# Kernel optimization log

Measured on AMD Instinct MI355X. Metric: run time of the kernel, lower is better.

## Reference

```python
import jax, jax.numpy as jnp
import numpy as np

DIM = 256
HEADS = 8
HEAD_DIM = DIM // HEADS
WS = 7            # window size
SHIFT = 3         # shift size
H = 56
W = 56
B = 32
WA = WS * WS      # window area = 49
NWH, NWW = H // WS, W // WS
NW = NWH * NWW    # windows per image


def _make_attn_mask():
    # replicate the torch mask construction for the shifted windows
    img = np.zeros((H, W), dtype=np.float32)
    cnt = 0
    for hs in (slice(0, -WS), slice(-WS, -SHIFT), slice(-SHIFT, None)):
        for ws_ in (slice(0, -WS), slice(-WS, -SHIFT), slice(-SHIFT, None)):
            img[hs, ws_] = cnt
            cnt += 1
    mw = img.reshape(NWH, WS, NWW, WS).transpose(0, 2, 1, 3).reshape(-1, WA)  # (nW, 49)
    diff = mw[:, None, :] - mw[:, :, None]                                    # (nW, 49, 49)
    return np.where(diff != 0, -100.0, 0.0).astype(np.float32)


def _make_rel_index():
    coords = np.stack(np.meshgrid(np.arange(WS), np.arange(WS), indexing='ij')).reshape(2, -1)
    rel = coords[:, :, None] - coords[:, None, :]        # (2, 49, 49)
    rel = rel.transpose(1, 2, 0) + (WS - 1)              # shift to >= 0
    rel[..., 0] *= 2 * WS - 1
    return rel.sum(-1).astype(np.int32)                  # (49, 49) in [0, 169)


def setup_inputs() -> dict:
    key = jax.random.key(0)
    ks = jax.random.split(key, 12)
    s = 0.02
    inp = {
        'x': jax.random.normal(ks[0], (B, H, W, DIM), dtype=jnp.float32),
        'ln1_w': jnp.ones((DIM,), jnp.float32), 'ln1_b': jnp.zeros((DIM,), jnp.float32),
        'qkv_w': s * jax.random.normal(ks[1], (3 * DIM, DIM), jnp.float32),
        'qkv_b': jnp.zeros((3 * DIM,), jnp.float32),
        'rpb_table': s * jax.random.normal(ks[2], ((2 * WS - 1) ** 2, HEADS), jnp.float32),
        'proj_w': s * jax.random.normal(ks[3], (DIM, DIM), jnp.float32),
        'proj_b': jnp.zeros((DIM,), jnp.float32),
        'ln2_w': jnp.ones((DIM,), jnp.float32), 'ln2_b': jnp.zeros((DIM,), jnp.float32),
        'fc1_w': s * jax.random.normal(ks[4], (4 * DIM, DIM), jnp.float32),
        'fc1_b': jnp.zeros((4 * DIM,), jnp.float32),
        'ln3_w': jnp.ones((4 * DIM,), jnp.float32), 'ln3_b': jnp.zeros((4 * DIM,), jnp.float32),
        'fc2_w': s * jax.random.normal(ks[5], (DIM, 4 * DIM), jnp.float32),
        'fc2_b': jnp.zeros((DIM,), jnp.float32),
        'attn_mask': jnp.asarray(_make_attn_mask()),     # (nW, 49, 49)
        'rel_index': jnp.asarray(_make_rel_index()),     # (49, 49) int32
    }
    return inp


def _ln(x, w, b, eps=1e-5):
    m = jnp.mean(x, axis=-1, keepdims=True)
    v = jnp.mean((x - m) ** 2, axis=-1, keepdims=True)
    return (x - m) * jax.lax.rsqrt(v + eps) * w + b


def reference(x, ln1_w, ln1_b, qkv_w, qkv_b, rpb_table, proj_w, proj_b,
              ln2_w, ln2_b, fc1_w, fc1_b, ln3_w, ln3_b, fc2_w, fc2_b,
              attn_mask, rel_index):
    Bn, Hn, Wn, C = x.shape
    # ---- attention branch ----
    y = _ln(x, ln1_w, ln1_b)
    sh = jnp.roll(y, (-SHIFT, -SHIFT), axis=(1, 2))
    # window partition: (B, H, W, C) -> (B*nW, 49, C)
    win = sh.reshape(Bn, NWH, WS, NWW, WS, C).transpose(0, 1, 3, 2, 4, 5).reshape(Bn * NW, WA, C)
    qkv = win @ qkv_w.T + qkv_b                              # (Bw, 49, 3C)
    qkv = qkv.reshape(Bn * NW, WA, 3, HEADS, HEAD_DIM).transpose(2, 0, 3, 1, 4)
    q, k, v = qkv[0], qkv[1], qkv[2]                         # (Bw, h, 49, d)
    scale = HEAD_DIM ** -0.5
    attn = jnp.einsum('bhqd,bhkd->bhqk', q * scale, k)       # (Bw, h, 49, 49)
    bias = rpb_table[rel_index]                              # (49, 49, h)
    attn = attn + jnp.transpose(bias, (2, 0, 1))[None]
    attn = attn.reshape(Bn, NW, HEADS, WA, WA) + attn_mask[None, :, None]
    attn = jax.nn.softmax(attn, axis=-1).reshape(Bn * NW, HEADS, WA, WA)
    out = jnp.einsum('bhqk,bhkd->bhqd', attn, v)             # (Bw, h, 49, d)
    out = out.transpose(0, 2, 1, 3).reshape(Bn * NW, WA, C)
    out = out @ proj_w.T + proj_b
    # window reverse + un-shift
    out = out.reshape(Bn, NWH, NWW, WS, WS, C).transpose(0, 1, 3, 2, 4, 5).reshape(Bn, Hn, Wn, C)
    out = jnp.roll(out, (SHIFT, SHIFT), axis=(1, 2))
    x = x + out
    # ---- MLP branch (note: extra LayerNorm inside MLP per source) ----
    z = _ln(x, ln2_w, ln2_b)
    h = jax.nn.gelu(z @ fc1_w.T + fc1_b, approximate=False)
    h = _ln(h, ln3_w, ln3_b)
    x = x + (h @ fc2_w.T + fc2_b)
    return x
```

## Files before the change

kernel.cpp:

```cpp
#include <hip/hip_runtime.h>
#include <hip/hip_bf16.h>
#include <math.h>

typedef __attribute__((ext_vector_type(8))) short bf16x8;
typedef __attribute__((ext_vector_type(4))) float f32x4;
typedef __attribute__((ext_vector_type(4))) float f4;
typedef __attribute__((ext_vector_type(8))) unsigned short us8;
typedef __attribute__((ext_vector_type(4))) unsigned short us4;
typedef unsigned short u16;
typedef unsigned int u32;

#define HEADS 8
#define SHIFT_ 3
#define HIMG 56
#define WIMG 56
#define WA 49
#define NTOK 100352
#define NPAIR 16384

static __device__ __forceinline__ float bf2f(u16 v){ return __uint_as_float(((u32)v)<<16); }
static __device__ __forceinline__ u16 f2bf(float f){
  u32 u = __float_as_uint(f);
  return (u16)((u + 0x7fffu + ((u>>16)&1u)) >> 16);
}
static __device__ __forceinline__ u32 pkbf(float a, float b){
  __hip_bfloat162 h = __float22bfloat162_rn(make_float2(a, b));
  return *reinterpret_cast<u32*>(&h);
}
static __device__ __forceinline__ float wsum(float v){
  #pragma unroll
  for (int off=32; off>0; off>>=1) v += __shfl_xor(v, off, 64);
  return v;
}
static __device__ __forceinline__ void glds16(const u16* g, u16* l){
  __builtin_amdgcn_global_load_lds(
      (const __attribute__((address_space(1))) unsigned int*)g,
      (__attribute__((address_space(3))) unsigned int*)l, 16, 0, 0);
}
static __device__ __forceinline__ int tok2pix(int row){
  int bw = row / 49, t = row - bw*49;
  int b  = bw >> 6,  w = bw & 63;
  int wh = w >> 3,   ww = w & 7;
  int th = t / 7,    tw = t - th*7;
  int r = wh*7 + th + SHIFT_; if (r >= HIMG) r -= HIMG;
  int c = ww*7 + tw + SHIFT_; if (c >= WIMG) c -= WIMG;
  return (b*HIMG + r)*WIMG + c;
}
static __device__ __forceinline__ float gelu_f(float x){
  float e = __expf(-1.702f*x);
  return x*__builtin_amdgcn_rcpf(1.0f+e);
}

__global__ void zero_kernel(float* __restrict__ p){
  p[blockIdx.x*256 + threadIdx.x] = 0.f;
}

template<int C, int ISBF>
__global__ void ln_stats_kernel(const void* __restrict__ srcv, float* __restrict__ stats){
  int wave = threadIdx.x >> 6, lane = threadIdx.x & 63;
  int tok = blockIdx.x*4 + wave;
  float s=0.f, s2=0.f;
  if (ISBF == 0){
    const float* p = (const float*)srcv + (size_t)tok*C;
    #pragma unroll
    for (int i=0;i<C/256;i++){
      f4 v = *(const f4*)(p + lane*4*(C/256) + i*4);
      #pragma unroll
      for (int e=0;e<4;e++){ float f=v[e]; s+=f; s2+=f*f; }
    }
  } else {
    const u16* p = (const u16*)srcv + (size_t)tok*C;
    #pragma unroll
    for (int i=0;i<C/512;i++){
      us8 v = *(const us8*)(p + lane*8*(C/512) + i*8);
      #pragma unroll
      for (int e=0;e<8;e++){ float f=bf2f(v[e]); s+=f; s2+=f*f; }
    }
  }
  s = wsum(s); s2 = wsum(s2);
  if (lane==0){
    float mean = s/(float)C;
    float var  = s2/(float)C - mean*mean;
    stats[2*tok]   = mean;
    stats[2*tok+1] = rsqrtf(var + 1e-5f);
  }
}

__global__ void ln_apply_kernel(const float* __restrict__ src, u16* __restrict__ dst){
  int wave = threadIdx.x >> 6, lane = threadIdx.x & 63;
  int tok = blockIdx.x*4 + wave;
  const float* p = src + (size_t)tok*256;
  f4 a = *(const f4*)(p + lane*4);
  float s = a[0]+a[1]+a[2]+a[3];
  float s2 = a[0]*a[0]+a[1]*a[1]+a[2]*a[2]+a[3]*a[3];
  s = wsum(s); s2 = wsum(s2);
  float mean = s*(1.f/256.f);
  float var  = s2*(1.f/256.f) - mean*mean;
  float rstd = rsqrtf(var + 1e-5f);
  u32 o2[2];
  o2[0] = pkbf((a[0]-mean)*rstd, (a[1]-mean)*rstd);
  o2[1] = pkbf((a[2]-mean)*rstd, (a[3]-mean)*rstd);
  *(u32*)(dst + (size_t)tok*256 + lane*4)     = o2[0];
  *(u32*)(dst + (size_t)tok*256 + lane*4 + 2) = o2[1];
}

__global__ void ln_apply_b_kernel(const u16* __restrict__ src, u16* __restrict__ dst,
                                  float* __restrict__ st){
  int wave = threadIdx.x >> 6, lane = threadIdx.x & 63;
  int tok = blockIdx.x*4 + wave;
  const u16* p = src + (size_t)tok*256 + lane*4;
  us4 a4 = *(const us4*)p;
  float a0=bf2f(a4[0]), a1=bf2f(a4[1]), a2=bf2f(a4[2]), a3=bf2f(a4[3]);
  float s = a0+a1+a2+a3;
  float s2 = a0*a0+a1*a1+a2*a2+a3*a3;
  s = wsum(s); s2 = wsum(s2);
  float mean = s*(1.f/256.f);
  float var  = s2*(1.f/256.f) - mean*mean;
  float rstd = rsqrtf(var + 1e-5f);
  u32 o0 = pkbf((a0-mean)*rstd, (a1-mean)*rstd);
  u32 o1 = pkbf((a2-mean)*rstd, (a3-mean)*rstd);
  u16* d = dst + (size_t)tok*256 + lane*4;
  *(u32*)d     = o0;
  *(u32*)(d+2) = o1;
  if (lane==0){ st[2*tok] = mean; st[2*tok+1] = rstd; }
}

__global__ void prep_weights(
    const float* __restrict__ qkv_w, const float* __restrict__ qkv_b,
    const float* __restrict__ ln1w,  const float* __restrict__ ln1b,
    const float* __restrict__ fc1_w, const float* __restrict__ fc1_b,
    const float* __restrict__ ln2w,  const float* __restrict__ ln2b,
    const float* __restrict__ fc2_w, const float* __restrict__ fc2_b,
    const float* __restrict__ ln3w,  const float* __restrict__ ln3b,
    const float* __restrict__ proj_w, const float* __restrict__ proj_b,
    u16* __restrict__ wq, float* __restrict__ bq,
    u16* __restrict__ w1, float* __restrict__ b1,
    u16* __restrict__ w2, float* __restrict__ b2,
    u16* __restrict__ wp, float* __restrict__ bp,
    float* __restrict__ cs2)
{
  int wave = threadIdx.x>>6, lane = threadIdx.x&63;
  int n = blockIdx.x*4 + wave;
  const float *W,*lw,*lb,*bs; u16* WO; float* BO; int K, row, noln, docs;
  if (n < 768)      { W=qkv_w; lw=ln1w; lb=ln1b; bs=qkv_b; WO=wq; BO=bq; K=256;  row=n;      noln=0; docs=0; }
  else if (n < 1792){ W=fc1_w; lw=ln2w; lb=ln2b; bs=fc1_b; WO=w1; BO=b1; K=256;  row=n-768;  noln=0; docs=0; }
  else if (n < 2048){ W=fc2_w; lw=ln3w; lb=ln3b; bs=fc2_b; WO=w2; BO=b2; K=1024; row=n-1792; noln=0; docs=1; }
  else              { W=proj_w; lw=nullptr; lb=nullptr; bs=proj_b; WO=wp; BO=bp; K=256; row=n-2048; noln=1; docs=0; }
  float dot = 0.f, cs = 0.f;
  for (int k=lane; k<K; k+=64){
    float wv = W[(size_t)row*K + k];
    if (noln){
      WO[(size_t)row*K + k] = f2bf(wv);
    } else {
      dot += wv * lb[k];
      u16 q = f2bf(wv * lw[k]);
      WO[(size_t)row*K + k] = q;
      cs += bf2f(q);
    }
  }
  dot = wsum(dot);
  if (docs){ cs = wsum(cs); if (lane==0) cs2[row] = cs; }
  if (lane==0) BO[row] = bs[row] + dot;
}

template<int SMODE, int EPI, int SWAP>
__global__ __launch_bounds__(256)
void gemm17(const void* __restrict__ Av, const u16* __restrict__ Bt,
            const float* __restrict__ stats, float* __restrict__ hstats,
            const float* __restrict__ biasf, const float* __restrict__ resid,
            const float* __restrict__ colsum, void* __restrict__ outv,
            int K, int NT, int CHUNK)
{
  constexpr int BM=128, BN=128, BK=32;
  __shared__ u16 smem[24576];
  int b = blockIdx.x;
  int linear = (b & 7)*CHUNK + (b >> 3);
  int mt = linear / NT, nt = linear - mt*NT;
  int m0 = mt*BM, n0 = nt*BN;
  int tid  = threadIdx.x;
  int lane = tid & 63, wave = tid >> 6;
  int wr = wave >> 1, wc = wave & 1;
  int lc16 = lane & 15, g = lane >> 4;
  int nsteps = K >> 5;

  const u16* asrc[2];
  const u16* bsrc[2];
  #pragma unroll
  for (int i=0;i<2;i++){
    int c = tid + i*256;
    int row = c >> 2, gch = ((c & 3) - (row >> 1)) & 3;
    if (SMODE <= 1){
      int grow = (SMODE==0) ? tok2pix(m0+row) : (m0+row);
      asrc[i] = (const u16*)Av + (size_t)grow*K + gch*8;
    }
    bsrc[i] = Bt + (size_t)(n0+row)*K + gch*8;
  }
  float smean[2], srstd[2];
  if (SMODE == 3){
    #pragma unroll
    for (int i=0;i<2;i++){
      int grow = m0 + ((tid + i*256) >> 2);
      smean[i] = stats[2*grow]; srstd[i] = stats[2*grow+1];
    }
  }

  f32x4 acc[4][4];
  #pragma unroll
  for (int i=0;i<4;i++)
    #pragma unroll
    for (int j=0;j<4;j++){ acc[i][j][0]=0.f; acc[i][j][1]=0.f; acc[i][j][2]=0.f; acc[i][j][3]=0.f; }

  if (SMODE <= 1){
    #pragma unroll
    for (int i=0;i<2;i++) glds16(asrc[i], smem + i*2048 + wave*512);
    #pragma unroll
    for (int i=0;i<2;i++) glds16(bsrc[i], smem + 12288 + i*2048 + wave*512);
    if (1 < nsteps){
      #pragma unroll
      for (int i=0;i<2;i++) glds16(asrc[i]+32, smem + 4096 + i*2048 + wave*512);
      #pragma unroll
      for (int i=0;i<2;i++) glds16(bsrc[i]+32, smem + 12288 + 4096 + i*2048 + wave*512);
      asm volatile("s_waitcnt vmcnt(4)" ::: "memory");
    } else {
      asm volatile("s_waitcnt vmcnt(0)" ::: "memory");
    }
    __builtin_amdgcn_s_barrier();

    int cur = 0;
    for (int t=0; t<nsteps; ++t){
      if (t+2 < nsteps){
        int kt2 = (t+2) << 5;
        int nb = cur + 2; if (nb >= 3) nb -= 3;
        int off = nb*4096;
        #pragma unroll
        for (int i=0;i<2;i++) glds16(asrc[i]+kt2, smem + off + i*2048 + wave*512);
        #pragma unroll
        for (int i=0;i<2;i++) glds16(bsrc[i]+kt2, smem + 12288 + off + i*2048 + wave*512);
      }
      const u16* Ap = smem + cur*4096;
      const u16* Bp = smem + 12288 + cur*4096;
      bf16x8 af[4], bfr[4];
      #pragma unroll
      for (int mi=0;mi<4;mi++){
        int r = wr*64 + mi*16 + lc16;
        u32 byte = (u32)(r*64) + ((u32)((g + (r>>1)) & 3) << 4);
        af[mi] = *(const bf16x8*)(Ap + (byte>>1));
      }
      #pragma unroll
      for (int ni=0;ni<4;ni++){
        int r = wc*64 + ni*16 + lc16;
        u32 byte = (u32)(r*64) + ((u32)((g + (r>>1)) & 3) << 4);
        bfr[ni] = *(const bf16x8*)(Bp + (byte>>1));
      }
      #pragma unroll
      for (int mi=0;mi<4;mi++)
        #pragma unroll
        for (int ni=0;ni<4;ni++)
          acc[mi][ni] = SWAP ? __builtin_amdgcn_mfma_f32_16x16x32_bf16(bfr[ni], af[mi], acc[mi][ni], 0, 0, 0)
                             : __builtin_amdgcn_mfma_f32_16x16x32_bf16(af[mi], bfr[ni], acc[mi][ni], 0, 0, 0);
      if (t+2 < nsteps)      asm volatile("s_waitcnt vmcnt(4)" ::: "memory");
      else if (t+1 < nsteps) asm volatile("s_waitcnt vmcnt(0)" ::: "memory");
      __builtin_amdgcn_s_barrier();
      cur = (cur+1 == 3) ? 0 : cur+1;
    }
  } else {
    f4 rcurf[2][2];
    #pragma unroll
    for (int i=0;i<2;i++){
      int c = tid + i*256; int row = c>>2, gch = ((c&3) - (row>>1)) & 3;
      const float* ap = (const float*)Av + (size_t)(m0+row)*K + gch*8;
      rcurf[i][0] = *(const f4*)ap; rcurf[i][1] = *(const f4*)(ap+4);
    }
    for (int t=0; t<nsteps; ++t){
      int kt = t << 5;
      #pragma unroll
      for (int i=0;i<2;i++){
        int c = tid + i*256; int row = c>>2, s = c&3;
        us8 o;
        #pragma unroll
        for (int e=0;e<8;e++){
          float fv = rcurf[i][e>>2][e&3];
          o[e] = f2bf((fv - smean[i])*srstd[i]);
        }
        u32 byte = (u32)(row*64) + ((u32)s << 4);
        *(us8*)(smem + (byte>>1)) = o;
      }
      #pragma unroll
      for (int i=0;i<2;i++) glds16(bsrc[i]+kt, smem + 12288 + i*2048 + wave*512);
      __syncthreads();
      if (t+1 < nsteps){
        int kt1 = kt + 32;
        #pragma unroll
        for (int i=0;i<2;i++){
          int c = tid + i*256; int row = c>>2, gch = ((c&3) - (row>>1)) & 3;
          const float* ap = (const float*)Av + (size_t)(m0+row)*K + kt1 + gch*8;
          rcurf[i][0] = *(const f4*)ap; rcurf[i][1] = *(const f4*)(ap+4);
        }
      }
      bf16x8 af[4], bfr[4];
      #pragma unroll
      for (int mi=0;mi<4;mi++){
        int r = wr*64 + mi*16 + lc16;
        u32 byte = (u32)(r*64) + ((u32)((g + (r>>1)) & 3) << 4);
        af[mi] = *(const bf16x8*)(smem + (byte>>1));
      }
      #pragma unroll
      for (int ni=0;ni<4;ni++){
        int r = wc*64 + ni*16 + lc16;
        u32 byte = (u32)(r*64) + ((u32)((g + (r>>1)) & 3) << 4);
        bfr[ni] = *(const bf16x8*)(smem + 12288 + (byte>>1));
      }
      #pragma unroll
      for (int mi=0;mi<4;mi++)
        #pragma unroll
        for (int ni=0;ni<4;ni++)
          acc[mi][ni] = SWAP ? __builtin_amdgcn_mfma_f32_16x16x32_bf16(bfr[ni], af[mi], acc[mi][ni], 0, 0, 0)
                             : __builtin_amdgcn_mfma_f32_16x16x32_bf16(af[mi], bfr[ni], acc[mi][ni], 0, 0, 0);
      __syncthreads();
    }
  }

  int lr = lane >> 4;
  if (EPI==0){
    u16* Cs = smem;
    #pragma unroll
    for (int mi=0;mi<4;mi++){
      #pragma unroll
      for (int ni=0;ni<4;ni++){
        int cl = wc*64 + ni*16 + lc16;
        float bv = biasf[n0 + cl];
        #pragma unroll
        for (int j=0;j<4;j++){
          int rl = wr*64 + mi*16 + lr*4 + j;
          float v = acc[mi][ni][j] + bv;
          u32 byte = (u32)(rl*256 + cl*2) ^ ((u32)(rl&7)<<4);
          Cs[byte>>1] = f2bf(v);
        }
      }
    }
    __syncthreads();
    #pragma unroll
    for (int i=0;i<8;i++){
      int c = tid + i*256;
      int rl = c>>4, c0 = (c&15)*8;
      u32 byte = (u32)(rl*256 + c0*2) ^ ((u32)(rl&7)<<4);
      us8 v = *(const us8*)(Cs + (byte>>1));
      int row = m0 + rl, col = n0 + c0;
      int which = col>>8, hh = (col>>5)&7, d0 = col&31;
      int bwi = row/49, t = row - bwi*49;
      *(us8*)((u16*)outv + ((size_t)which*NPAIR + bwi*8 + hh)*(WA*32) + t*32 + d0) = v;
    }
  } else if (EPI==2){
    u16* Cs = smem;
    #pragma unroll
    for (int mi=0;mi<4;mi++){
      int rl = wr*64 + mi*16 + lc16;
      float ss = 0.f, sq = 0.f;
      #pragma unroll
      for (int ni=0;ni<4;ni++){
        int cl = wc*64 + ni*16 + g*4;
        f4 bv = *(const f4*)(biasf + n0 + cl);
        float v0 = gelu_f(acc[mi][ni][0] + bv[0]);
        float v1 = gelu_f(acc[mi][ni][1] + bv[1]);
        float v2 = gelu_f(acc[mi][ni][2] + bv[2]);
        float v3 = gelu_f(acc[mi][ni][3] + bv[3]);
        ss += (v0+v1)+(v2+v3);
        sq += (v0*v0+v1*v1)+(v2*v2+v3*v3);
        u32 w0 = pkbf(v0, v1), w1 = pkbf(v2, v3);
        u32 byte = (u32)(rl*256 + cl*2) ^ ((u32)(rl&7)<<4);
        *(u32*)(Cs + (byte>>1))     = w0;
        *(u32*)(Cs + (byte>>1) + 2) = w1;
      }
      ss += __shfl_xor(ss, 16, 64); ss += __shfl_xor(ss, 32, 64);
      sq += __shfl_xor(sq, 16, 64); sq += __shfl_xor(sq, 32, 64);
      if (g==0){
        int grow = m0 + rl;
        atomicAdd(&hstats[2*grow],   ss);
        atomicAdd(&hstats[2*grow+1], sq);
      }
    }
    __syncthreads();
    #pragma unroll
    for (int i=0;i<8;i++){
      int c = tid + i*256;
      int rl = c>>4, c0 = (c&15)*8;
      u32 byte = (u32)(rl*256 + c0*2) ^ ((u32)(rl&7)<<4);
      us8 v = *(const us8*)(Cs + (byte>>1));
      int row = m0 + rl, col = n0 + c0;
      *(us8*)((u16*)outv + (size_t)row*1024 + col) = v;
    }
  } else if (EPI==5){
    u16* Cs = smem;
    #pragma unroll
    for (int mi=0;mi<4;mi++){
      int rl = wr*64 + mi*16 + lc16;
      int pix = tok2pix(m0 + rl);
      #pragma unroll
      for (int ni=0;ni<4;ni++){
        int cl = wc*64 + ni*16 + g*4;
        int col = n0 + cl;
        f4 bv = *(const f4*)(biasf + col);
        f4 rr = *(const f4*)(resid + (size_t)pix*256 + col);
        float v0 = acc[mi][ni][0] + bv[0] + rr[0];
        float v1 = acc[mi][ni][1] + bv[1] + rr[1];
        float v2 = acc[mi][ni][2] + bv[2] + rr[2];
        float v3 = acc[mi][ni][3] + bv[3] + rr[3];
        u32 w0 = pkbf(v0, v1), w1 = pkbf(v2, v3);
        u32 byte = (u32)(rl*256 + cl*2) ^ ((u32)(rl&7)<<4);
        *(u32*)(Cs + (byte>>1))     = w0;
        *(u32*)(Cs + (byte>>1) + 2) = w1;
      }
    }
    __syncthreads();
    #pragma unroll
    for (int i=0;i<8;i++){
      int c = tid + i*256;
      int rl = c>>4, c0 = (c&15)*8;
      u32 byte = (u32)(rl*256 + c0*2) ^ ((u32)(rl&7)<<4);
      us8 v = *(const us8*)(Cs + (byte>>1));
      int pix = tok2pix(m0 + rl);
      *(us8*)((u16*)outv + (size_t)pix*256 + n0 + c0) = v;
    }
  } else {
    #pragma unroll
    for (int mi=0;mi<4;mi++){
      int rl = wr*64 + mi*16 + lc16;
      int grow = m0 + rl;
      float rs = 1.f, mr = 0.f, istd2 = 0.f, mean2 = 0.f;
      if (EPI==4 || EPI==6){
        float s = stats[2*grow], q = stats[2*grow+1];
        float mean = s*(1.f/1024.f);
        float var  = q*(1.f/1024.f) - mean*mean;
        rs = rsqrtf(var + 1e-5f);
        mr = mean*rs;
      }
      if (EPI==6){
        mean2 = hstats[2*grow];
        istd2 = __builtin_amdgcn_rcpf(hstats[2*grow+1]);
      }
      size_t rowbase = (EPI==1) ? (size_t)tok2pix(grow)*256 : (size_t)grow*256;
      #pragma unroll
      for (int ni=0;ni<4;ni++){
        int col = n0 + wc*64 + ni*16 + g*4;
        f4 bv = *(const f4*)(biasf + col);
        f4 v;
        if (EPI==4 || EPI==6){
          f4 cw = *(const f4*)(colsum + col);
          #pragma unroll
          for (int j=0;j<4;j++) v[j] = acc[mi][ni][j]*rs - mr*cw[j] + bv[j];
        } else {
          #pragma unroll
          for (int j=0;j<4;j++) v[j] = acc[mi][ni][j] + bv[j];
        }
        if (EPI==6){
          us4 xr = *(const us4*)((const u16*)resid + rowbase + col);
          #pragma unroll
          for (int j=0;j<4;j++) v[j] += bf2f(xr[j])*istd2 + mean2;
        } else {
          f4 rr = *(const f4*)(resid + rowbase + col);
          v += rr;
        }
        *(f4*)((float*)outv + rowbase + col) = v;
      }
    }
  }
}

__global__ void attn_mfma_kernel(
    const u16* __restrict__ qkv,
    const float* __restrict__ rpb,
    const int* __restrict__ rel,
    const float* __restrict__ mask,
    u16* __restrict__ outb)
{
  __shared__ u16 Kls[4][64*32];
  __shared__ u16 Vt [4][32*64];
  __shared__ u16 Pls[4][64*64];
  int wave = threadIdx.x>>6, lane = threadIdx.x&63;
  int pair = blockIdx.x*4 + wave;
  int bw = pair>>3, h = pair&7, w = bw&63;
  int lc = lane&15, g = lane>>4;
  const u16* qg = qkv + (size_t)pair*(WA*32);
  const u16* kg = qg + (size_t)NPAIR*(WA*32);
  const u16* vg = qg + (size_t)2*NPAIR*(WA*32);
  u16* Kp = &Kls[wave][0];
  u16* Vp = &Vt[wave][0];
  u16* Pp = &Pls[wave][0];

  #pragma unroll
  for (int i=0;i<4;i++){
    int idx = i*64 + lane;
    int r = idx>>2, seg = idx&3;
    us8 kv, vv;
    if (r < WA){
      kv = *(const us8*)(kg + r*32 + seg*8);
      vv = *(const us8*)(vg + r*32 + seg*8);
    } else {
      #pragma unroll
      for (int e=0;e<8;e++){ kv[e]=0; vv[e]=0; }
    }
    *(us8*)(Kp + r*32 + seg*8) = kv;
    #pragma unroll
    for (int e=0;e<8;e++){
      int d = seg*8 + e;
      u32 byte = ((u32)(d*128 + r*2)) ^ ((u32)(d&7)<<4);
      Vp[byte>>1] = vv[e];
    }
  }

  bf16x8 qa[4];
  #pragma unroll
  for (int mi=0;mi<4;mi++){
    int r = mi*16 + lc;
    if (r < WA) qa[mi] = *(const bf16x8*)(qg + r*32 + g*8);
    else { bf16x8 z;
           #pragma unroll
           for (int e=0;e<8;e++) z[e]=0; qa[mi]=z; }
  }

  f32x4 acc[4][4];
  #pragma unroll
  for (int i=0;i<4;i++)
    #pragma unroll
    for (int j=0;j<4;j++){ acc[i][j][0]=0.f; acc[i][j][1]=0.f; acc[i][j][2]=0.f; acc[i][j][3]=0.f; }
  __syncthreads();
  __builtin_amdgcn_s_setprio(1);
  #pragma unroll
  for (int ni=0;ni<4;ni++){
    bf16x8 kb = *(const bf16x8*)(Kp + (ni*16+lc)*32 + g*8);
    #pragma unroll
    for (int mi=0;mi<4;mi++)
      acc[mi][ni] = __builtin_amdgcn_mfma_f32_16x16x32_bf16(qa[mi], kb, acc[mi][ni], 0, 0, 0);
  }
  __builtin_amdgcn_s_setprio(0);

  const float scale = 0.17677669529663689f;
  float rinv[4][4];
  #pragma unroll
  for (int mi=0;mi<4;mi++){
    #pragma unroll
    for (int jr=0;jr<4;jr++){
      int i = mi*16 + g*4 + jr;
      float sv[4];
      #pragma unroll
      for (int ni=0;ni<4;ni++){
        int j = ni*16 + lc;
        float s;
        if (i < WA && j < WA){
          s = acc[mi][ni][jr]*scale + rpb[rel[i*WA+j]*8 + h] + mask[((size_t)w*WA + i)*WA + j];
        } else s = -1e9f;
        sv[ni] = s;
      }
      float mx = fmaxf(fmaxf(sv[0],sv[1]), fmaxf(sv[2],sv[3]));
      #pragma unroll
      for (int off=1; off<16; off<<=1) mx = fmaxf(mx, __shfl_xor(mx, off, 64));
      float sum = 0.f;
      #pragma unroll
      for (int ni=0;ni<4;ni++){ sv[ni] = __expf(sv[ni]-mx); sum += sv[ni]; }
      #pragma unroll
      for (int off=1; off<16; off<<=1) sum += __shfl_xor(sum, off, 64);
      rinv[mi][jr] = __builtin_amdgcn_rcpf(sum);
      #pragma unroll
      for (int ni=0;ni<4;ni++){
        int j = ni*16 + lc;
        u32 byte = ((u32)(i*128 + j*2)) ^ ((u32)(i&7)<<4);
        Pp[byte>>1] = f2bf(sv[ni]);
      }
    }
  }

  bf16x8 vb[2][2];
  #pragma unroll
  for (int kk=0;kk<2;kk++)
    #pragma unroll
    for (int ni=0;ni<2;ni++){
      int d = ni*16 + lc;
      u32 byte = ((u32)(d*128 + kk*64 + g*16)) ^ ((u32)(d&7)<<4);
      vb[kk][ni] = *(const bf16x8*)(Vp + (byte>>1));
    }
  f32x4 aco[4][2];
  #pragma unroll
  for (int i=0;i<4;i++)
    #pragma unroll
    for (int j=0;j<2;j++){ aco[i][j][0]=0.f; aco[i][j][1]=0.f; aco[i][j][2]=0.f; aco[i][j][3]=0.f; }
  __builtin_amdgcn_s_setprio(1);
  #pragma unroll
  for (int mi=0;mi<4;mi++){
    int r = mi*16 + lc;
    #pragma unroll
    for (int kk=0;kk<2;kk++){
      u32 byte = ((u32)(r*128 + kk*64 + g*16)) ^ ((u32)(r&7)<<4);
      bf16x8 pa = *(const bf16x8*)(Pp + (byte>>1));
      #pragma unroll
      for (int ni=0;ni<2;ni++)
        aco[mi][ni] = __builtin_amdgcn_mfma_f32_16x16x32_bf16(pa, vb[kk][ni], aco[mi][ni], 0, 0, 0);
    }
  }
  __builtin_amdgcn_s_setprio(0);

  u16* Op = Kp;
  #pragma unroll
  for (int mi=0;mi<4;mi++){
    #pragma unroll
    for (int jr=0;jr<4;jr++){
      int i = mi*16 + g*4 + jr;
      if (i < WA){
        float rv = rinv[mi][jr];
        #pragma unroll
        for (int ni=0;ni<2;ni++)
          Op[i*32 + ni*16 + lc] = f2bf(aco[mi][ni][jr]*rv);
      }
    }
  }
  __syncthreads();
  size_t obase = (size_t)(bw*WA)*256 + h*32;
  #pragma unroll
  for (int i=0;i<4;i++){
    int c = i*64 + lane;
    if (c < WA*4){
      int t = c>>2, seg = c&3;
      *(us8*)(outb + obase + (size_t)t*256 + seg*8) = *(const us8*)(Op + t*32 + seg*8);
    }
  }
}

extern "C" void kernel_launch(void* const* d_in, const int* in_sizes, int n_in,
                              void* d_out, int out_size, void* d_ws, size_t ws_size,
                              hipStream_t stream) {
  const float* x      = (const float*)d_in[0];
  const float* ln1w   = (const float*)d_in[1];
  const float* ln1b   = (const float*)d_in[2];
  const float* qkv_w  = (const float*)d_in[3];
  const float* qkv_b  = (const float*)d_in[4];
  const float* rpb    = (const float*)d_in[5];
  const float* proj_w = (const float*)d_in[6];
  const float* proj_b = (const float*)d_in[7];
  const float* ln2w   = (const float*)d_in[8];
  const float* ln2b   = (const float*)d_in[9];
  const float* fc1_w  = (const float*)d_in[10];
  const float* fc1_b  = (const float*)d_in[11];
  const float* ln3w   = (const float*)d_in[12];
  const float* ln3b   = (const float*)d_in[13];
  const float* fc2_w  = (const float*)d_in[14];
  const float* fc2_b  = (const float*)d_in[15];
  const float* amask  = (const float*)d_in[16];
  const int*   rel    = (const int*)d_in[17];
  float* out = (float*)d_out;

  char* ws = (char*)d_ws;
  float* hstats = (float*)(ws);
  float* stats2 = (float*)(ws +  802816);
  float* bq     = (float*)(ws + 1605632);
  float* b1     = (float*)(ws + 1608704);
  float* b2     = (float*)(ws + 1612800);
  float* bp     = (float*)(ws + 1613824);
  float* cs2    = (float*)(ws + 1614848);
  u16*   wq     = (u16*)  (ws + 1615872);
  u16*   w1     = (u16*)  (ws + 2009088);
  u16*   w2     = (u16*)  (ws + 2533376);
  u16*   wp     = (u16*)  (ws + 3057664);
  const size_t P0 = 3188736;
  u16*   qkvbuf = (u16*)(ws + P0);
  u16*   attno  = (u16*)(ws + P0 + 154140672);
  u16*   xb     = (u16*)(ws + P0 + 154140672);
  u16*   ob     = (u16*)(ws + P0);
  u16*   hbuf   = (u16*)(ws + P0);
  u16*   x1b    = (u16*)(ws + P0 + 205520896);
  const int bigws = (ws_size >= (size_t)(P0 + 205520896ull + 51380224ull));

  prep_weights<<<576,256,0,stream>>>(qkv_w,qkv_b,ln1w,ln1b, fc1_w,fc1_b,ln2w,ln2b,
                                     fc2_w,fc2_b,ln3w,ln3b, proj_w,proj_b,
                                     wq,bq, w1,b1, w2,b2, wp,bp, cs2);
  ln_apply_kernel<<<NTOK/4,256,0,stream>>>(x, xb);
  gemm17<0,0,0><<<784*6,256,0,stream>>>(xb, wq, nullptr, nullptr, bq, nullptr, nullptr, qkvbuf, 256, 6, 588);
  attn_mfma_kernel<<<NPAIR/4,256,0,stream>>>(qkvbuf, rpb, rel, amask, attno);
  zero_kernel<<<784,256,0,stream>>>(hstats);
  if (bigws){
    gemm17<1,5,1><<<784*2,256,0,stream>>>(attno, wp, nullptr, nullptr, bp, x, nullptr, ob, 256, 2, 196);
    ln_apply_b_kernel<<<NTOK/4,256,0,stream>>>(ob, x1b, stats2);
    gemm17<1,2,1><<<784*8,256,0,stream>>>(x1b, w1, nullptr, hstats, b1, nullptr, nullptr, hbuf, 256, 8, 784);
    gemm17<1,6,1><<<784*2,256,0,stream>>>(hbuf, w2, hstats, stats2, b2, (const float*)x1b, cs2, out, 1024, 2, 196);
  } else {
    gemm17<1,1,1><<<784*2,256,0,stream>>>(attno, wp, nullptr, nullptr, bp, x, nullptr, out, 256, 2, 196);
    ln_stats_kernel<256,0><<<NTOK/4,256,0,stream>>>(out, stats2);
    gemm17<3,2,1><<<784*8,256,0,stream>>>(out, w1, stats2, hstats, b1, nullptr, nullptr, (u16*)(ws+P0), 256, 8, 784);
    gemm17<1,4,1><<<784*2,256,0,stream>>>((u16*)(ws+P0), w2, hstats, nullptr, b2, out, cs2, out, 1024, 2, 196);
  }
}
```

Measured before the change: 531.9 us.

## Parameterize GEMM prefetch depth, fold q scale into weights, merge zeroing

Templates the GEMM on a prefetch depth and uses a 4-buffer, depth-3 global-to-LDS pipeline for the K=1024 fc2 GEMM, so more loads are in flight to hide memory latency. The attention softmax scale is folded into the q rows of the QKV weights and bias during weight prep, which removes a multiply per score. The separate hstats zero kernel is merged into prep_weights to save a launch. The cost is larger LDS use per block (64KB for the depth-3 GEMM), which may lower occupancy, and a slight bf16 rounding difference from pre-scaling q.

```diff
diff --git a/kernel.cpp b/kernel.cpp
--- a/kernel.cpp
+++ b/kernel.cpp
@@ -49,10 +49,6 @@
 static __device__ __forceinline__ float gelu_f(float x){
   float e = __expf(-1.702f*x);
   return x*__builtin_amdgcn_rcpf(1.0f+e);
-}
-
-__global__ void zero_kernel(float* __restrict__ p){
-  p[blockIdx.x*256 + threadIdx.x] = 0.f;
 }
 
 template<int C, int ISBF>
@@ -137,12 +133,17 @@
     u16* __restrict__ w1, float* __restrict__ b1,
     u16* __restrict__ w2, float* __restrict__ b2,
     u16* __restrict__ wp, float* __restrict__ bp,
-    float* __restrict__ cs2)
+    float* __restrict__ cs2, float* __restrict__ hstats)
 {
+  for (int idx = blockIdx.x*256 + threadIdx.x; idx < 2*NTOK; idx += gridDim.x*256)
+    hstats[idx] = 0.f;
+
   int wave = threadIdx.x>>6, lane = threadIdx.x&63;
   int n = blockIdx.x*4 + wave;
   const float *W,*lw,*lb,*bs; u16* WO; float* BO; int K, row, noln, docs;
-  if (n < 768)      { W=qkv_w; lw=ln1w; lb=ln1b; bs=qkv_b; WO=wq; BO=bq; K=256;  row=n;      noln=0; docs=0; }
+  float qs = 1.f;
+  if (n < 768)      { W=qkv_w; lw=ln1w; lb=ln1b; bs=qkv_b; WO=wq; BO=bq; K=256;  row=n;      noln=0; docs=0;
+                      if (n < 256) qs = 0.17677669529663689f; }
   else if (n < 1792){ W=fc1_w; lw=ln2w; lb=ln2b; bs=fc1_b; WO=w1; BO=b1; K=256;  row=n-768;  noln=0; docs=0; }
   else if (n < 2048){ W=fc2_w; lw=ln3w; lb=ln3b; bs=fc2_b; WO=w2; BO=b2; K=1024; row=n-1792; noln=0; docs=1; }
   else              { W=proj_w; lw=nullptr; lb=nullptr; bs=proj_b; WO=wp; BO=bp; K=256; row=n-2048; noln=1; docs=0; }
@@ -153,26 +154,28 @@
       WO[(size_t)row*K + k] = f2bf(wv);
     } else {
       dot += wv * lb[k];
-      u16 q = f2bf(wv * lw[k]);
+      u16 q = f2bf(wv * lw[k] * qs);
       WO[(size_t)row*K + k] = q;
       cs += bf2f(q);
     }
   }
   dot = wsum(dot);
   if (docs){ cs = wsum(cs); if (lane==0) cs2[row] = cs; }
-  if (lane==0) BO[row] = bs[row] + dot;
-}
-
-template<int SMODE, int EPI, int SWAP>
+  if (lane==0) BO[row] = (bs[row] + dot) * qs;
+}
+
+template<int SMODE, int EPI, int SWAP, int DEPTH>
 __global__ __launch_bounds__(256)
-void gemm17(const void* __restrict__ Av, const u16* __restrict__ Bt,
+void gemm18(const void* __restrict__ Av, const u16* __restrict__ Bt,
             const float* __restrict__ stats, float* __restrict__ hstats,
             const float* __restrict__ biasf, const float* __restrict__ resid,
             const float* __restrict__ colsum, void* __restrict__ outv,
             int K, int NT, int CHUNK)
 {
   constexpr int BM=128, BN=128, BK=32;
-  __shared__ u16 smem[24576];
+  constexpr int NBUF = DEPTH + 1;
+  __shared__ u16 smem[NBUF*8192];
+  constexpr int BOFF = NBUF*4096;
   int b = blockIdx.x;
   int linear = (b & 7)*CHUNK + (b >> 3);
   int mt = linear / NT, nt = linear - mt*NT;
@@ -212,33 +215,30 @@
 
   if (SMODE <= 1){
     #pragma unroll
-    for (int i=0;i<2;i++) glds16(asrc[i], smem + i*2048 + wave*512);
-    #pragma unroll
-    for (int i=0;i<2;i++) glds16(bsrc[i], smem + 12288 + i*2048 + wave*512);
-    if (1 < nsteps){
-      #pragma unroll
-      for (int i=0;i<2;i++) glds16(asrc[i]+32, smem + 4096 + i*2048 + wave*512);
-      #pragma unroll
-      for (int i=0;i<2;i++) glds16(bsrc[i]+32, smem + 12288 + 4096 + i*2048 + wave*512);
-      asm volatile("s_waitcnt vmcnt(4)" ::: "memory");
-    } else {
-      asm volatile("s_waitcnt vmcnt(0)" ::: "memory");
-    }
+    for (int pt=0; pt<DEPTH; ++pt){
+      int kt = pt << 5;
+      #pragma unroll
+      for (int i=0;i<2;i++) glds16(asrc[i]+kt, smem + pt*4096 + i*2048 + wave*512);
+      #pragma unroll
+      for (int i=0;i<2;i++) glds16(bsrc[i]+kt, smem + BOFF + pt*4096 + i*2048 + wave*512);
+    }
+    if (DEPTH == 3)      asm volatile("s_waitcnt vmcnt(8)" ::: "memory");
+    else                 asm volatile("s_waitcnt vmcnt(4)" ::: "memory");
     __builtin_amdgcn_s_barrier();
 
     int cur = 0;
     for (int t=0; t<nsteps; ++t){
-      if (t+2 < nsteps){
-        int kt2 = (t+2) << 5;
-        int nb = cur + 2; if (nb >= 3) nb -= 3;
+      if (t+DEPTH < nsteps){
+        int ktD = (t+DEPTH) << 5;
+        int nb = cur + DEPTH; if (nb >= NBUF) nb -= NBUF;
         int off = nb*4096;
         #pragma unroll
-        for (int i=0;i<2;i++) glds16(asrc[i]+kt2, smem + off + i*2048 + wave*512);
-        #pragma unroll
-        for (int i=0;i<2;i++) glds16(bsrc[i]+kt2, smem + 12288 + off + i*2048 + wave*512);
+        for (int i=0;i<2;i++) glds16(asrc[i]+ktD, smem + off + i*2048 + wave*512);
+        #pragma unroll
+        for (int i=0;i<2;i++) glds16(bsrc[i]+ktD, smem + BOFF + off + i*2048 + wave*512);
       }
       const u16* Ap = smem + cur*4096;
-      const u16* Bp = smem + 12288 + cur*4096;
+      const u16* Bp = smem + BOFF + cur*4096;
       bf16x8 af[4], bfr[4];
       #pragma unroll
       for (int mi=0;mi<4;mi++){
@@ -258,10 +258,13 @@
         for (int ni=0;ni<4;ni++)
           acc[mi][ni] = SWAP ? __builtin_amdgcn_mfma_f32_16x16x32_bf16(bfr[ni], af[mi], acc[mi][ni], 0, 0, 0)
                              : __builtin_amdgcn_mfma_f32_16x16x32_bf16(af[mi], bfr[ni], acc[mi][ni], 0, 0, 0);
-      if (t+2 < nsteps)      asm volatile("s_waitcnt vmcnt(4)" ::: "memory");
-      else if (t+1 < nsteps) asm volatile("s_waitcnt vmcnt(0)" ::: "memory");
+      int rem = nsteps - 1 - t;
+      int cnt = (rem < DEPTH) ? rem : DEPTH;
+      if (cnt >= 3)      asm volatile("s_waitcnt vmcnt(8)" ::: "memory");
+      else if (cnt == 2) asm volatile("s_waitcnt vmcnt(4)" ::: "memory");
+      else if (cnt == 1) asm volatile("s_waitcnt vmcnt(0)" ::: "memory");
       __builtin_amdgcn_s_barrier();
-      cur = (cur+1 == 3) ? 0 : cur+1;
+      cur = (cur+1 == NBUF) ? 0 : cur+1;
     }
   } else {
     f4 rcurf[2][2];
@@ -286,7 +289,7 @@
         *(us8*)(smem + (byte>>1)) = o;
       }
       #pragma unroll
-      for (int i=0;i<2;i++) glds16(bsrc[i]+kt, smem + 12288 + i*2048 + wave*512);
+      for (int i=0;i<2;i++) glds16(bsrc[i]+kt, smem + BOFF + i*2048 + wave*512);
       __syncthreads();
       if (t+1 < nsteps){
         int kt1 = kt + 32;
@@ -308,7 +311,7 @@
       for (int ni=0;ni<4;ni++){
         int r = wc*64 + ni*16 + lc16;
         u32 byte = (u32)(r*64) + ((u32)((g + (r>>1)) & 3) << 4);
-        bfr[ni] = *(const bf16x8*)(smem + 12288 + (byte>>1));
+        bfr[ni] = *(const bf16x8*)(smem + BOFF + (byte>>1));
       }
       #pragma unroll
       for (int mi=0;mi<4;mi++)
@@ -534,7 +537,6 @@
   }
   __builtin_amdgcn_s_setprio(0);
 
-  const float scale = 0.17677669529663689f;
   float rinv[4][4];
   #pragma unroll
   for (int mi=0;mi<4;mi++){
@@ -547,7 +549,7 @@
         int j = ni*16 + lc;
         float s;
         if (i < WA && j < WA){
-          s = acc[mi][ni][jr]*scale + rpb[rel[i*WA+j]*8 + h] + mask[((size_t)w*WA + i)*WA + j];
+          s = acc[mi][ni][jr] + rpb[rel[i*WA+j]*8 + h] + mask[((size_t)w*WA + i)*WA + j];
         } else s = -1e9f;
         sv[ni] = s;
       }
@@ -670,20 +672,19 @@
 
   prep_weights<<<576,256,0,stream>>>(qkv_w,qkv_b,ln1w,ln1b, fc1_w,fc1_b,ln2w,ln2b,
                                      fc2_w,fc2_b,ln3w,ln3b, proj_w,proj_b,
-                                     wq,bq, w1,b1, w2,b2, wp,bp, cs2);
+                                     wq,bq, w1,b1, w2,b2, wp,bp, cs2, hstats);
   ln_apply_kernel<<<NTOK/4,256,0,stream>>>(x, xb);
-  gemm17<0,0,0><<<784*6,256,0,stream>>>(xb, wq, nullptr, nullptr, bq, nullptr, nullptr, qkvbuf, 256, 6, 588);
+  gemm18<0,0,0,2><<<784*6,256,0,stream>>>(xb, wq, nullptr, nullptr, bq, nullptr, nullptr, qkvbuf, 256, 6, 588);
   attn_mfma_kernel<<<NPAIR/4,256,0,stream>>>(qkvbuf, rpb, rel, amask, attno);
-  zero_kernel<<<784,256,0,stream>>>(hstats);
   if (bigws){
-    gemm17<1,5,1><<<784*2,256,0,stream>>>(attno, wp, nullptr, nullptr, bp, x, nullptr, ob, 256, 2, 196);
+    gemm18<1,5,1,2><<<784*2,256,0,stream>>>(attno, wp, nullptr, nullptr, bp, x, nullptr, ob, 256, 2, 196);
     ln_apply_b_kernel<<<NTOK/4,256,0,stream>>>(ob, x1b, stats2);
-    gemm17<1,2,1><<<784*8,256,0,stream>>>(x1b, w1, nullptr, hstats, b1, nullptr, nullptr, hbuf, 256, 8, 784);
-    gemm17<1,6,1><<<784*2,256,0,stream>>>(hbuf, w2, hstats, stats2, b2, (const float*)x1b, cs2, out, 1024, 2, 196);
+    gemm18<1,2,1,2><<<784*8,256,0,stream>>>(x1b, w1, nullptr, hstats, b1, nullptr, nullptr, hbuf, 256, 8, 784);
+    gemm18<1,6,1,3><<<784*2,256,0,stream>>>(hbuf, w2, hstats, stats2, b2, (const float*)x1b, cs2, out, 1024, 2, 196);
   } else {
-    gemm17<1,1,1><<<784*2,256,0,stream>>>(attno, wp, nullptr, nullptr, bp, x, nullptr, out, 256, 2, 196);
+    gemm18<1,1,1,2><<<784*2,256,0,stream>>>(attno, wp, nullptr, nullptr, bp, x, nullptr, out, 256, 2, 196);
     ln_stats_kernel<256,0><<<NTOK/4,256,0,stream>>>(out, stats2);
-    gemm17<3,2,1><<<784*8,256,0,stream>>>(out, w1, stats2, hstats, b1, nullptr, nullptr, (u16*)(ws+P0), 256, 8, 784);
-    gemm17<1,4,1><<<784*2,256,0,stream>>>((u16*)(ws+P0), w2, hstats, nullptr, b2, out, cs2, out, 1024, 2, 196);
-  }
-}
+    gemm18<3,2,1,2><<<784*8,256,0,stream>>>(out, w1, stats2, hstats, b1, nullptr, nullptr, (u16*)(ws+P0), 256, 8, 784);
+    gemm18<1,4,1,2><<<784*2,256,0,stream>>>((u16*)(ws+P0), w2, hstats, nullptr, b2, out, cs2, out, 1024, 2, 196);
+  }
+}
```

After: 527.8 us. No clear change (-0.8%).
